# Kernel tuning notes

Hardware: AMD Instinct MI355X
Metric: run time of the kernel (lower is better)

The kernel has to match this reference:

```python
import jax, jax.numpy as jnp
import numpy as np

EPS = 1e-5


def setup_inputs() -> dict:
    key = jax.random.key(0)
    k1, k2, k3 = jax.random.split(key, 3)
    B, D, T = 16, 256, 4096
    K = 2048
    x = jax.random.normal(k1, (B, D, T), dtype=jnp.float32)
    embedding_sum = jax.random.normal(k2, (K, D), dtype=jnp.float32)
    cluster_usage = jax.random.uniform(k3, (K,), dtype=jnp.float32)
    return {"x": x, "embedding_sum": embedding_sum, "cluster_usage": cluster_usage}


def reference(x, embedding_sum, cluster_usage):
    # embedding property: embedding_sum / clamp(cluster_usage, min=eps)
    emb = embedding_sum / jnp.clip(cluster_usage, EPS, None)[:, None]  # [K, D]
    B, D, T = x.shape
    x_flat = jnp.transpose(x, (0, 2, 1)).reshape(B * T, D)  # (b t) d
    # compute faithfully (clamped for numerical safety).
    x2 = jnp.sum(x_flat * x_flat, axis=-1, keepdims=True)      # [BT, 1]
    e2 = jnp.sum(emb * emb, axis=-1)                           # [K]
    d2 = x2 - 2.0 * (x_flat @ emb.T) + e2[None, :]             # [BT, K]
    distances = jnp.sqrt(jnp.clip(d2, 0.0, None))
    codes = jnp.argmin(distances, axis=-1).reshape(B, 1, T)    # int codes
    # decode: embedding gather, b t d -> b d t
    decoded = jnp.transpose(emb[codes[:, 0, :]], (0, 2, 1))    # [B, D, T]
    return codes, decoded
```

## Files before the change

kernel.cpp:

```cpp
#include <hip/hip_runtime.h>
#include <hip/hip_fp16.h>
#include <cmath>

#define EPS 1e-5f
#define TAU 0.15f
#define RP  8

#define Bn 16
#define Dn 256
#define Tn 4096
#define Kn 2048

typedef unsigned short ushort_t;
typedef __attribute__((ext_vector_type(8))) _Float16 f16x8;
typedef __attribute__((ext_vector_type(4))) float f32x4;

__device__ __forceinline__ unsigned short f2h(float v) {
    return __half_as_ushort(__float2half_rn(v));
}

#define GLOAD_LDS16(gp, lp) __builtin_amdgcn_global_load_lds( \
    (const __attribute__((address_space(1))) unsigned int*)(gp), \
    (__attribute__((address_space(3))) unsigned int*)(lp), 16, 0, 0)

__global__ __launch_bounds__(256) void prep_kernel(
    const float* __restrict__ es, const float* __restrict__ usage,
    float* __restrict__ emb, ushort_t* __restrict__ e16,
    float* __restrict__ bias, float4* __restrict__ embT4,
    int* __restrict__ counter)
{
    __shared__ float sh[256];
    __shared__ float wsum[4];
    const int k = blockIdx.x;
    const int d = threadIdx.x;
    const float inv = 1.0f / fmaxf(usage[k], EPS);
    const float v = es[(size_t)k * Dn + d] * inv;
    emb[(size_t)k * Dn + d] = v;
    e16[(size_t)k * Dn + d] = f2h(fminf(fmaxf(v, -65504.f), 65504.f));
    sh[d] = v;
    float sq = v * v;
    #pragma unroll
    for (int off = 32; off > 0; off >>= 1) sq += __shfl_down(sq, off, 64);
    const int lane = d & 63, wv = d >> 6;
    if (lane == 0) wsum[wv] = sq;
    __syncthreads();
    if (d < 64)
        embT4[(size_t)d * Kn + k] = make_float4(sh[4*d], sh[4*d+1], sh[4*d+2], sh[4*d+3]);
    if (d == 0) {
        bias[k] = 0.5f * (wsum[0] + wsum[1] + wsum[2] + wsum[3]);
        if (k == 0) *counter = 0;
    }
}

#define BARRIER_PIN()                                                         \
    __builtin_amdgcn_s_barrier();                                             \
    __builtin_amdgcn_sched_barrier(0)

#define STAGE_B(dst, kcc, hh)                                                 \
    {                                                                         \
        _Pragma("unroll")                                                     \
        for (int r = 0; r < 4; ++r) {                                         \
            const int c   = r * 512 + tid;                                    \
            const int row = c >> 4;                                           \
            const int col = (((c & 15) ^ (row & 15)) << 3);                   \
            GLOAD_LDS16(e16 + ((size_t)((kcc) * 128 + row)) * Dn + (hh) * 128 + col, \
                        (dst) + ((r * 512 + (wid << 6)) << 3));               \
        }                                                                     \
    }

#define COMPUTE_ACC(bbuf, afArr)                                              \
    {                                                                         \
        __builtin_amdgcn_s_setprio(1);                                        \
        _Pragma("unroll")                                                     \
        for (int ks = 0; ks < 4; ++ks)                                        \
            _Pragma("unroll")                                                 \
            for (int j = 0; j < 8; ++j) {                                     \
                const f16x8 bf = *(const f16x8*)(                             \
                    &(bbuf)[((j << 4) + l15) * 128 +                          \
                            ((((ks << 2) | quad) ^ l15) << 3)]);              \
                _Pragma("unroll")                                             \
                for (int i = 0; i < 2; ++i)                                   \
                    acc[i][j] = __builtin_amdgcn_mfma_f32_16x16x32_f16(       \
                        afArr[ks * 2 + i], bf, acc[i][j], 0, 0, 0);           \
            }                                                                 \
        __builtin_amdgcn_s_setprio(0);                                        \
    }

__global__ __launch_bounds__(512, 2) void gemm_argmax(
    const float* __restrict__ x, const ushort_t* __restrict__ e16,
    const float* __restrict__ bias_g, int* __restrict__ codes_i,
    float* __restrict__ codes_f, int* __restrict__ list,
    int* __restrict__ counter)
{
    __shared__ __align__(16) ushort_t BsS[2][128 * 128];
    __shared__ __align__(16) float    biasLds[2048];

    const int bid = blockIdx.x;
    const int b   = bid >> 4;
    const int tt  = bid & 15;
    const int t0  = tt << 8;

    const int tid  = threadIdx.x;
    const int lane = tid & 63;
    const int wid  = tid >> 6;
    const int l15  = lane & 15;
    const int quad = lane >> 4;
    const int wm   = wid;

    const size_t bTt0 = (size_t)b * Tn + t0;

    GLOAD_LDS16(bias_g + (tid << 2), biasLds + (wid << 8));

    f16x8 af0[8], af1[8];
    {
        const float* xb = x + (size_t)b * Dn * Tn;
        #pragma unroll
        for (int ks = 0; ks < 4; ++ks)
            #pragma unroll
            for (int i = 0; i < 2; ++i) {
                const int t = t0 + (wm << 5) + (i << 4) + l15;
                const float* c0 = xb + ((size_t)(ks * 32 + quad * 8)) * Tn + t;
                const float* c1 = c0 + (size_t)128 * Tn;
                f16x8 v0, v1;
                #pragma unroll
                for (int e = 0; e < 8; ++e) {
                    v0[e] = (_Float16)c0[(size_t)e * Tn];
                    v1[e] = (_Float16)c1[(size_t)e * Tn];
                }
                af0[ks * 2 + i] = v0;
                af1[ks * 2 + i] = v1;
            }
    }

    f32x4 acc[2][8];
    float S1[2][4], S2[2][4];
    int   K1[2][4];
    #pragma unroll
    for (int i = 0; i < 2; ++i)
        #pragma unroll
        for (int r = 0; r < 4; ++r) { S1[i][r] = -INFINITY; S2[i][r] = -INFINITY; K1[i][r] = 0; }
    #pragma unroll
    for (int i = 0; i < 2; ++i)
        #pragma unroll
        for (int j = 0; j < 8; ++j)
            acc[i][j] = (f32x4){-INFINITY, -INFINITY, -INFINITY, -INFINITY};

    asm volatile("s_waitcnt vmcnt(0)" ::: "memory");
    BARRIER_PIN();
    STAGE_B(&BsS[0][0], 0, 0);
    STAGE_B(&BsS[1][0], 0, 1);

    #pragma unroll 1
    for (int kc = 0; kc < 16; ++kc) {
        asm volatile("s_waitcnt vmcnt(4)" ::: "memory");
        BARRIER_PIN();
        {
            float bj[8];
            #pragma unroll
            for (int j = 0; j < 8; ++j)
                bj[j] = biasLds[(kc << 7) + (j << 4) + l15];
            const int kdrb = ((kc - 1) << 7) + l15;
            __builtin_amdgcn_s_setprio(1);
            #pragma unroll
            for (int j = 0; j < 8; ++j) {
                const f16x8 bf0 = *(const f16x8*)(
                    &BsS[0][((j << 4) + l15) * 128 + ((quad ^ l15) << 3)]);
                const float nb = -bj[j];
                const f32x4 cin = {nb, nb, nb, nb};
                const int kdr = kdrb + (j << 4);
                #pragma unroll
                for (int i = 0; i < 2; ++i) {
                    #pragma unroll
                    for (int r = 0; r < 4; ++r) {
                        const float s = acc[i][j][r];
                        S2[i][r] = __builtin_amdgcn_fmed3f(s, S1[i][r], S2[i][r]);
                        const bool gt = s > S1[i][r];
                        K1[i][r] = gt ? kdr : K1[i][r];
                        S1[i][r] = fmaxf(S1[i][r], s);
                    }
                    acc[i][j] = __builtin_amdgcn_mfma_f32_16x16x32_f16(
                        af0[i], bf0, cin, 0, 0, 0);
                }
            }
            #pragma unroll
            for (int ks = 1; ks < 4; ++ks)
                #pragma unroll
                for (int j = 0; j < 8; ++j) {
                    const f16x8 bf = *(const f16x8*)(
                        &BsS[0][((j << 4) + l15) * 128 +
                                ((((ks << 2) | quad) ^ l15) << 3)]);
                    #pragma unroll
                    for (int i = 0; i < 2; ++i)
                        acc[i][j] = __builtin_amdgcn_mfma_f32_16x16x32_f16(
                            af0[ks * 2 + i], bf, acc[i][j], 0, 0, 0);
                }
            __builtin_amdgcn_s_setprio(0);
        }
        BARRIER_PIN();
        if (kc < 15) STAGE_B(&BsS[0][0], kc + 1, 0);

        if (kc < 15) { asm volatile("s_waitcnt vmcnt(4)" ::: "memory"); }
        else         { asm volatile("s_waitcnt vmcnt(0)" ::: "memory"); }
        BARRIER_PIN();
        COMPUTE_ACC((&BsS[1][0]), af1);
        BARRIER_PIN();
        if (kc < 15) STAGE_B(&BsS[1][0], kc + 1, 1);
    }

    __builtin_amdgcn_sched_barrier(0);

    {
        const int kfb = (15 << 7) + l15;
        #pragma unroll
        for (int j = 0; j < 8; ++j) {
            const int kf = kfb + (j << 4);
            #pragma unroll
            for (int i = 0; i < 2; ++i)
                #pragma unroll
                for (int r = 0; r < 4; ++r) {
                    const float s = acc[i][j][r];
                    S2[i][r] = __builtin_amdgcn_fmed3f(s, S1[i][r], S2[i][r]);
                    const bool gt = s > S1[i][r];
                    K1[i][r] = gt ? kf : K1[i][r];
                    S1[i][r] = fmaxf(S1[i][r], s);
                }
        }
    }

    #pragma unroll
    for (int m = 1; m <= 8; m <<= 1) {
        #pragma unroll
        for (int i = 0; i < 2; ++i)
            #pragma unroll
            for (int r = 0; r < 4; ++r) {
                const float os1 = __shfl_xor(S1[i][r], m);
                const float os2 = __shfl_xor(S2[i][r], m);
                const int   ok1 = __shfl_xor(K1[i][r], m);
                const bool take = (os1 > S1[i][r]) || (os1 == S1[i][r] && ok1 < K1[i][r]);
                const float ns2 = take ? fmaxf(S1[i][r], os2) : fmaxf(S2[i][r], os1);
                if (take) { S1[i][r] = os1; K1[i][r] = ok1; }
                S2[i][r] = ns2;
            }
    }

    if (l15 == 0) {
        #pragma unroll
        for (int i = 0; i < 2; ++i)
            #pragma unroll
            for (int r = 0; r < 4; ++r) {
                const int row = (wm << 5) + (i << 4) + (quad << 2) + r;
                const size_t p = bTt0 + row;
                const int wk = K1[i][r];
                codes_i[p] = wk;
                codes_f[p] = (float)wk;
                if (S1[i][r] - S2[i][r] < TAU) {
                    const int idx = atomicAdd(counter, 1);
                    list[idx] = (int)p;
                }
            }
    }
}

__global__ __launch_bounds__(256) void rescue_kernel(
    const float* __restrict__ x, const float4* __restrict__ embT4,
    const float* __restrict__ bias, const int* __restrict__ list,
    const int* __restrict__ counter, int* __restrict__ codes_i,
    float* __restrict__ codes_f)
{
    __shared__ float xv[RP][256];
    __shared__ int plist[RP];
    __shared__ float rs[RP][4];
    __shared__ int   rk[RP][4];
    const int tid = threadIdx.x, lane = tid & 63, wid = tid >> 6;
    const int count = *counter;
    for (int base = blockIdx.x * RP; base < count; base += gridDim.x * RP) {
        const int npts = min(RP, count - base);
        __syncthreads();
        if (tid < npts) plist[tid] = list[base + tid];
        __syncthreads();
        for (int pi = 0; pi < npts; ++pi) {
            const int p = plist[pi];
            xv[pi][tid] = x[((size_t)((p >> 12) * Dn + tid)) * Tn + (p & 4095)];
        }
        for (int pi = npts; pi < RP; ++pi) xv[pi][tid] = 0.f;
        __syncthreads();

        float acc[8][RP];
        #pragma unroll
        for (int s = 0; s < 8; ++s)
            #pragma unroll
            for (int pi = 0; pi < RP; ++pi) acc[s][pi] = 0.f;

        for (int dc = 0; dc < 64; ++dc) {
            float4 ev[8];
            #pragma unroll
            for (int s = 0; s < 8; ++s)
                ev[s] = embT4[(size_t)dc * Kn + tid + (s << 8)];
            #pragma unroll
            for (int pi = 0; pi < RP; ++pi) {
                const float4 xw = *(const float4*)&xv[pi][dc << 2];
                #pragma unroll
                for (int s = 0; s < 8; ++s)
                    acc[s][pi] += ev[s].x * xw.x + ev[s].y * xw.y
                                + ev[s].z * xw.z + ev[s].w * xw.w;
            }
        }

        float bs[RP]; int bk[RP];
        #pragma unroll
        for (int pi = 0; pi < RP; ++pi) { bs[pi] = -INFINITY; bk[pi] = 0; }
        #pragma unroll
        for (int s = 0; s < 8; ++s) {
            const int kk = tid + (s << 8);
            const float bv = bias[kk];
            #pragma unroll
            for (int pi = 0; pi < RP; ++pi) {
                const float sc = acc[s][pi] - bv;
                if (sc > bs[pi]) { bs[pi] = sc; bk[pi] = kk; }
            }
        }
        #pragma unroll
        for (int off = 1; off < 64; off <<= 1) {
            #pragma unroll
            for (int pi = 0; pi < RP; ++pi) {
                const float os = __shfl_xor(bs[pi], off);
                const int   ok = __shfl_xor(bk[pi], off);
                if (os > bs[pi] || (os == bs[pi] && ok < bk[pi])) { bs[pi] = os; bk[pi] = ok; }
            }
        }
        if (lane == 0) {
            #pragma unroll
            for (int pi = 0; pi < RP; ++pi) { rs[pi][wid] = bs[pi]; rk[pi][wid] = bk[pi]; }
        }
        __syncthreads();
        if (tid < npts) {
            float fs = rs[tid][0]; int fk = rk[tid][0];
            #pragma unroll
            for (int w = 1; w < 4; ++w) {
                if (rs[tid][w] > fs || (rs[tid][w] == fs && rk[tid][w] < fk)) {
                    fs = rs[tid][w]; fk = rk[tid][w];
                }
            }
            const int p = plist[tid];
            codes_i[p] = fk;
            codes_f[p] = (float)fk;
        }
    }
}

__global__ __launch_bounds__(256) void decode_kernel(
    const float* __restrict__ emb, const int* __restrict__ codes,
    float* __restrict__ out)
{
    const int b = blockIdx.y;
    const int t = blockIdx.x * 256 + threadIdx.x;
    const int c = codes[(size_t)b * Tn + t];
    const float4* e4 = (const float4*)(emb + (size_t)c * Dn);
    float* ob = out + (size_t)b * Dn * Tn + t;
    #pragma unroll 4
    for (int d4 = 0; d4 < 64; ++d4) {
        const float4 v = e4[d4];
        ob[(size_t)(d4 * 4 + 0) * Tn] = v.x;
        ob[(size_t)(d4 * 4 + 1) * Tn] = v.y;
        ob[(size_t)(d4 * 4 + 2) * Tn] = v.z;
        ob[(size_t)(d4 * 4 + 3) * Tn] = v.w;
    }
}

extern "C" void kernel_launch(void* const* d_in, const int* in_sizes, int n_in,
                              void* d_out, int out_size, void* d_ws, size_t ws_size,
                              hipStream_t stream) {
    const float* x     = (const float*)d_in[0];
    const float* es    = (const float*)d_in[1];
    const float* usage = (const float*)d_in[2];

    char* ws = (char*)d_ws;
    float*    emb     = (float*)(ws + 0);
    float*    bias    = (float*)(ws + 2097152);
    ushort_t* e16     = (ushort_t*)(ws + 2105344);
    float4*   embT4   = (float4*)(ws + 3153920);
    int*      codes_i = (int*)(ws + 5251072);
    int*      list    = (int*)(ws + 5513216);
    int*      counter = (int*)(ws + 5775360);

    float* codes_f = (float*)d_out;
    float* decoded = (float*)d_out + (size_t)Bn * Tn;

    prep_kernel<<<Kn, 256, 0, stream>>>(es, usage, emb, e16, bias, embT4, counter);

    gemm_argmax<<<256, 512, 0, stream>>>(x, e16, bias, codes_i, codes_f,
                                         list, counter);

    rescue_kernel<<<1024, 256, 0, stream>>>(x, embT4, bias, list, counter, codes_i, codes_f);

    dim3 g6(Tn / 256, Bn);
    decode_kernel<<<g6, 256, 0, stream>>>(emb, codes_i, decoded);
}
```

Baseline: 306.0 us.

## Halve GEMM row tile per block and split decode over D chunks

The fused GEMM+argmax kernel now gives each wave 16 token rows instead of 32. The grid doubles to 512 blocks of 128 tokens, and launch bounds are raised to allow more resident blocks per CU. The decode kernel gains a z dimension that splits the 256-wide D loop into four chunks for more parallelism. The aim is better CU occupancy and load balance. In exchange, each B tile staged in LDS is reused across half as many MMAs, which doubles the embedding traffic per token. LDS use per block (about 72KB) may also cap the real occupancy gain.

```diff
diff --git a/kernel.cpp b/kernel.cpp
--- a/kernel.cpp
+++ b/kernel.cpp
@@ -78,15 +78,13 @@
                 const f16x8 bf = *(const f16x8*)(                             \
                     &(bbuf)[((j << 4) + l15) * 128 +                          \
                             ((((ks << 2) | quad) ^ l15) << 3)]);              \
-                _Pragma("unroll")                                             \
-                for (int i = 0; i < 2; ++i)                                   \
-                    acc[i][j] = __builtin_amdgcn_mfma_f32_16x16x32_f16(       \
-                        afArr[ks * 2 + i], bf, acc[i][j], 0, 0, 0);           \
+                acc[j] = __builtin_amdgcn_mfma_f32_16x16x32_f16(              \
+                    afArr[ks], bf, acc[j], 0, 0, 0);                          \
             }                                                                 \
         __builtin_amdgcn_s_setprio(0);                                        \
     }
 
-__global__ __launch_bounds__(512, 2) void gemm_argmax(
+__global__ __launch_bounds__(512, 4) void gemm_argmax(
     const float* __restrict__ x, const ushort_t* __restrict__ e16,
     const float* __restrict__ bias_g, int* __restrict__ codes_i,
     float* __restrict__ codes_f, int* __restrict__ list,
@@ -96,9 +94,9 @@
     __shared__ __align__(16) float    biasLds[2048];
 
     const int bid = blockIdx.x;
-    const int b   = bid >> 4;
-    const int tt  = bid & 15;
-    const int t0  = tt << 8;
+    const int b   = bid >> 5;
+    const int tt  = bid & 31;
+    const int t0  = tt << 7;
 
     const int tid  = threadIdx.x;
     const int lane = tid & 63;
@@ -111,39 +109,33 @@
 
     GLOAD_LDS16(bias_g + (tid << 2), biasLds + (wid << 8));
 
-    f16x8 af0[8], af1[8];
+    f16x8 af0[4], af1[4];
     {
         const float* xb = x + (size_t)b * Dn * Tn;
-        #pragma unroll
-        for (int ks = 0; ks < 4; ++ks)
-            #pragma unroll
-            for (int i = 0; i < 2; ++i) {
-                const int t = t0 + (wm << 5) + (i << 4) + l15;
-                const float* c0 = xb + ((size_t)(ks * 32 + quad * 8)) * Tn + t;
-                const float* c1 = c0 + (size_t)128 * Tn;
-                f16x8 v0, v1;
-                #pragma unroll
-                for (int e = 0; e < 8; ++e) {
-                    v0[e] = (_Float16)c0[(size_t)e * Tn];
-                    v1[e] = (_Float16)c1[(size_t)e * Tn];
-                }
-                af0[ks * 2 + i] = v0;
-                af1[ks * 2 + i] = v1;
-            }
-    }
-
-    f32x4 acc[2][8];
-    float S1[2][4], S2[2][4];
-    int   K1[2][4];
+        const int t = t0 + (wm << 4) + l15;
+        #pragma unroll
+        for (int ks = 0; ks < 4; ++ks) {
+            const float* c0 = xb + ((size_t)(ks * 32 + quad * 8)) * Tn + t;
+            const float* c1 = c0 + (size_t)128 * Tn;
+            f16x8 v0, v1;
+            #pragma unroll
+            for (int e = 0; e < 8; ++e) {
+                v0[e] = (_Float16)c0[(size_t)e * Tn];
+                v1[e] = (_Float16)c1[(size_t)e * Tn];
+            }
+            af0[ks] = v0;
+            af1[ks] = v1;
+        }
+    }
+
+    f32x4 acc[8];
+    float S1[4], S2[4];
+    int   K1[4];
     #pragma unroll
-    for (int i = 0; i < 2; ++i)
-        #pragma unroll
-        for (int r = 0; r < 4; ++r) { S1[i][r] = -INFINITY; S2[i][r] = -INFINITY; K1[i][r] = 0; }
+    for (int r = 0; r < 4; ++r) { S1[r] = -INFINITY; S2[r] = -INFINITY; K1[r] = 0; }
     #pragma unroll
-    for (int i = 0; i < 2; ++i)
-        #pragma unroll
-        for (int j = 0; j < 8; ++j)
-            acc[i][j] = (f32x4){-INFINITY, -INFINITY, -INFINITY, -INFINITY};
+    for (int j = 0; j < 8; ++j)
+        acc[j] = (f32x4){-INFINITY, -INFINITY, -INFINITY, -INFINITY};
 
     asm volatile("s_waitcnt vmcnt(0)" ::: "memory");
     BARRIER_PIN();
@@ -169,18 +161,15 @@
                 const f32x4 cin = {nb, nb, nb, nb};
                 const int kdr = kdrb + (j << 4);
                 #pragma unroll
-                for (int i = 0; i < 2; ++i) {
-                    #pragma unroll
-                    for (int r = 0; r < 4; ++r) {
-                        const float s = acc[i][j][r];
-                        S2[i][r] = __builtin_amdgcn_fmed3f(s, S1[i][r], S2[i][r]);
-                        const bool gt = s > S1[i][r];
-                        K1[i][r] = gt ? kdr : K1[i][r];
-                        S1[i][r] = fmaxf(S1[i][r], s);
-                    }
-                    acc[i][j] = __builtin_amdgcn_mfma_f32_16x16x32_f16(
-                        af0[i], bf0, cin, 0, 0, 0);
+                for (int r = 0; r < 4; ++r) {
+                    const float s = acc[j][r];
+                    S2[r] = __builtin_amdgcn_fmed3f(s, S1[r], S2[r]);
+                    const bool gt = s > S1[r];
+                    K1[r] = gt ? kdr : K1[r];
+                    S1[r] = fmaxf(S1[r], s);
                 }
+                acc[j] = __builtin_amdgcn_mfma_f32_16x16x32_f16(
+                    af0[0], bf0, cin, 0, 0, 0);
             }
             #pragma unroll
             for (int ks = 1; ks < 4; ++ks)
@@ -189,10 +178,8 @@
                     const f16x8 bf = *(const f16x8*)(
                         &BsS[0][((j << 4) + l15) * 128 +
                                 ((((ks << 2) | quad) ^ l15) << 3)]);
-                    #pragma unroll
-                    for (int i = 0; i < 2; ++i)
-                        acc[i][j] = __builtin_amdgcn_mfma_f32_16x16x32_f16(
-                            af0[ks * 2 + i], bf, acc[i][j], 0, 0, 0);
+                    acc[j] = __builtin_amdgcn_mfma_f32_16x16x32_f16(
+                        af0[ks], bf, acc[j], 0, 0, 0);
                 }
             __builtin_amdgcn_s_setprio(0);
         }
@@ -215,49 +202,43 @@
         for (int j = 0; j < 8; ++j) {
             const int kf = kfb + (j << 4);
             #pragma unroll
-            for (int i = 0; i < 2; ++i)
-                #pragma unroll
-                for (int r = 0; r < 4; ++r) {
-                    const float s = acc[i][j][r];
-                    S2[i][r] = __builtin_amdgcn_fmed3f(s, S1[i][r], S2[i][r]);
-                    const bool gt = s > S1[i][r];
-                    K1[i][r] = gt ? kf : K1[i][r];
-                    S1[i][r] = fmaxf(S1[i][r], s);
-                }
+            for (int r = 0; r < 4; ++r) {
+                const float s = acc[j][r];
+                S2[r] = __builtin_amdgcn_fmed3f(s, S1[r], S2[r]);
+                const bool gt = s > S1[r];
+                K1[r] = gt ? kf : K1[r];
+                S1[r] = fmaxf(S1[r], s);
+            }
         }
     }
 
     #pragma unroll
     for (int m = 1; m <= 8; m <<= 1) {
         #pragma unroll
-        for (int i = 0; i < 2; ++i)
-            #pragma unroll
-            for (int r = 0; r < 4; ++r) {
-                const float os1 = __shfl_xor(S1[i][r], m);
-                const float os2 = __shfl_xor(S2[i][r], m);
-                const int   ok1 = __shfl_xor(K1[i][r], m);
-                const bool take = (os1 > S1[i][r]) || (os1 == S1[i][r] && ok1 < K1[i][r]);
-                const float ns2 = take ? fmaxf(S1[i][r], os2) : fmaxf(S2[i][r], os1);
-                if (take) { S1[i][r] = os1; K1[i][r] = ok1; }
-                S2[i][r] = ns2;
-            }
+        for (int r = 0; r < 4; ++r) {
+            const float os1 = __shfl_xor(S1[r], m);
+            const float os2 = __shfl_xor(S2[r], m);
+            const int   ok1 = __shfl_xor(K1[r], m);
+            const bool take = (os1 > S1[r]) || (os1 == S1[r] && ok1 < K1[r]);
+            const float ns2 = take ? fmaxf(S1[r], os2) : fmaxf(S2[r], os1);
+            if (take) { S1[r] = os1; K1[r] = ok1; }
+            S2[r] = ns2;
+        }
     }
 
     if (l15 == 0) {
         #pragma unroll
-        for (int i = 0; i < 2; ++i)
-            #pragma unroll
-            for (int r = 0; r < 4; ++r) {
-                const int row = (wm << 5) + (i << 4) + (quad << 2) + r;
-                const size_t p = bTt0 + row;
-                const int wk = K1[i][r];
-                codes_i[p] = wk;
-                codes_f[p] = (float)wk;
-                if (S1[i][r] - S2[i][r] < TAU) {
-                    const int idx = atomicAdd(counter, 1);
-                    list[idx] = (int)p;
-                }
-            }
+        for (int r = 0; r < 4; ++r) {
+            const int row = (wm << 4) + (quad << 2) + r;
+            const size_t p = bTt0 + row;
+            const int wk = K1[r];
+            codes_i[p] = wk;
+            codes_f[p] = (float)wk;
+            if (S1[r] - S2[r] < TAU) {
+                const int idx = atomicAdd(counter, 1);
+                list[idx] = (int)p;
+            }
+        }
     }
 }
 
@@ -354,11 +335,13 @@
 {
     const int b = blockIdx.y;
     const int t = blockIdx.x * 256 + threadIdx.x;
+    const int z16 = blockIdx.z * 16;
     const int c = codes[(size_t)b * Tn + t];
     const float4* e4 = (const float4*)(emb + (size_t)c * Dn);
     float* ob = out + (size_t)b * Dn * Tn + t;
     #pragma unroll 4
-    for (int d4 = 0; d4 < 64; ++d4) {
+    for (int q = 0; q < 16; ++q) {
+        const int d4 = z16 + q;
         const float4 v = e4[d4];
         ob[(size_t)(d4 * 4 + 0) * Tn] = v.x;
         ob[(size_t)(d4 * 4 + 1) * Tn] = v.y;
@@ -388,11 +371,11 @@
 
     prep_kernel<<<Kn, 256, 0, stream>>>(es, usage, emb, e16, bias, embT4, counter);
 
-    gemm_argmax<<<256, 512, 0, stream>>>(x, e16, bias, codes_i, codes_f,
+    gemm_argmax<<<512, 512, 0, stream>>>(x, e16, bias, codes_i, codes_f,
                                          list, counter);
 
     rescue_kernel<<<1024, 256, 0, stream>>>(x, embT4, bias, list, counter, codes_i, codes_f);
 
-    dim3 g6(Tn / 256, Bn);
+    dim3 g6(Tn / 256, Bn, 4);
     decode_kernel<<<g6, 256, 0, stream>>>(emb, codes_i, decoded);
 }
```

Result: slower. 402.1 us (+31.4%).

## Fuse decode gather into GEMM-argmax epilogue and rescue kernel

Applied to the files above, without the earlier changes.

Removes the separate decode kernel. Each GEMM block stages its 256 winning codes in LDS and writes the gathered embedding rows straight into the transposed decoded output. The rescue kernel then overwrites decoded columns for the points whose codes it corrected. This saves a kernel launch and a re-read of codes, at the cost of a longer GEMM epilogue and a double write for rescued points, which must be ordered correctly across kernels.

```diff
diff --git a/kernel.cpp b/kernel.cpp
--- a/kernel.cpp
+++ b/kernel.cpp
@@ -88,12 +88,14 @@
 
 __global__ __launch_bounds__(512, 2) void gemm_argmax(
     const float* __restrict__ x, const ushort_t* __restrict__ e16,
-    const float* __restrict__ bias_g, int* __restrict__ codes_i,
-    float* __restrict__ codes_f, int* __restrict__ list,
-    int* __restrict__ counter)
+    const float* __restrict__ bias_g, const float* __restrict__ emb,
+    int* __restrict__ codes_i, float* __restrict__ codes_f,
+    int* __restrict__ list, int* __restrict__ counter,
+    float* __restrict__ decoded)
 {
     __shared__ __align__(16) ushort_t BsS[2][128 * 128];
     __shared__ __align__(16) float    biasLds[2048];
+    __shared__ int codeLds[256];
 
     const int bid = blockIdx.x;
     const int b   = bid >> 4;
@@ -251,6 +253,7 @@
                 const int row = (wm << 5) + (i << 4) + (quad << 2) + r;
                 const size_t p = bTt0 + row;
                 const int wk = K1[i][r];
+                codeLds[row] = wk;
                 codes_i[p] = wk;
                 codes_f[p] = (float)wk;
                 if (S1[i][r] - S2[i][r] < TAU) {
@@ -259,18 +262,37 @@
                 }
             }
     }
+    __syncthreads();
+
+    {
+        const int p2 = tid & 255;
+        const int dh = tid >> 8;
+        const int c  = codeLds[p2];
+        const float4* e4 = (const float4*)(emb + (size_t)c * Dn) + dh * 32;
+        float* ob = decoded + ((size_t)(b * Dn + dh * 128)) * Tn + t0 + p2;
+        #pragma unroll 4
+        for (int q = 0; q < 32; ++q) {
+            const float4 v = e4[q];
+            ob[(size_t)(q * 4 + 0) * Tn] = v.x;
+            ob[(size_t)(q * 4 + 1) * Tn] = v.y;
+            ob[(size_t)(q * 4 + 2) * Tn] = v.z;
+            ob[(size_t)(q * 4 + 3) * Tn] = v.w;
+        }
+    }
 }
 
 __global__ __launch_bounds__(256) void rescue_kernel(
     const float* __restrict__ x, const float4* __restrict__ embT4,
-    const float* __restrict__ bias, const int* __restrict__ list,
-    const int* __restrict__ counter, int* __restrict__ codes_i,
-    float* __restrict__ codes_f)
+    const float* __restrict__ bias, const float* __restrict__ emb,
+    const int* __restrict__ list, const int* __restrict__ counter,
+    int* __restrict__ codes_i, float* __restrict__ codes_f,
+    float* __restrict__ decoded)
 {
     __shared__ float xv[RP][256];
     __shared__ int plist[RP];
     __shared__ float rs[RP][4];
     __shared__ int   rk[RP][4];
+    __shared__ int   fcode[RP];
     const int tid = threadIdx.x, lane = tid & 63, wid = tid >> 6;
     const int count = *counter;
     for (int base = blockIdx.x * RP; base < count; base += gridDim.x * RP) {
@@ -344,26 +366,15 @@
             const int p = plist[tid];
             codes_i[p] = fk;
             codes_f[p] = (float)fk;
-        }
-    }
-}
-
-__global__ __launch_bounds__(256) void decode_kernel(
-    const float* __restrict__ emb, const int* __restrict__ codes,
-    float* __restrict__ out)
-{
-    const int b = blockIdx.y;
-    const int t = blockIdx.x * 256 + threadIdx.x;
-    const int c = codes[(size_t)b * Tn + t];
-    const float4* e4 = (const float4*)(emb + (size_t)c * Dn);
-    float* ob = out + (size_t)b * Dn * Tn + t;
-    #pragma unroll 4
-    for (int d4 = 0; d4 < 64; ++d4) {
-        const float4 v = e4[d4];
-        ob[(size_t)(d4 * 4 + 0) * Tn] = v.x;
-        ob[(size_t)(d4 * 4 + 1) * Tn] = v.y;
-        ob[(size_t)(d4 * 4 + 2) * Tn] = v.z;
-        ob[(size_t)(d4 * 4 + 3) * Tn] = v.w;
+            fcode[tid] = fk;
+        }
+        __syncthreads();
+        for (int pi = 0; pi < npts; ++pi) {
+            const int p = plist[pi];
+            const int c = fcode[pi];
+            decoded[((size_t)((p >> 12) * Dn + tid)) * Tn + (p & 4095)] =
+                emb[(size_t)c * Dn + tid];
+        }
     }
 }
 
@@ -388,11 +399,9 @@
 
     prep_kernel<<<Kn, 256, 0, stream>>>(es, usage, emb, e16, bias, embT4, counter);
 
-    gemm_argmax<<<256, 512, 0, stream>>>(x, e16, bias, codes_i, codes_f,
-                                         list, counter);
-
-    rescue_kernel<<<1024, 256, 0, stream>>>(x, embT4, bias, list, counter, codes_i, codes_f);
-
-    dim3 g6(Tn / 256, Bn);
-    decode_kernel<<<g6, 256, 0, stream>>>(emb, codes_i, decoded);
+    gemm_argmax<<<256, 512, 0, stream>>>(x, e16, bias, emb, codes_i, codes_f,
+                                         list, counter, decoded);
+
+    rescue_kernel<<<1024, 256, 0, stream>>>(x, embT4, bias, emb, list, counter,
+                                            codes_i, codes_f, decoded);
 }
```

Result: faster. 296.7 us (-3.0%).
